# Kernel tuning notes

Measured on AMD Instinct MI355X. Metric: run time of the kernel, lower is better.

## Reference

```python
import jax, jax.numpy as jnp
import numpy as np

EPS = 1e-6     # vnn repo EPS used in VN nonlinearity / batchnorm norm
BN_EPS = 1e-5  # torch BatchNorm default eps
K = 40         # args.n_knn


def knn_idx(x, k):
    # x: (B, 3, N) -> (B, N, k) indices of k nearest neighbors (incl. self)
    inner = -2.0 * jnp.einsum('bdn,bdm->bnm', x, x)
    xx = jnp.sum(x * x, axis=1)  # (B, N)
    neg_dist = -xx[:, :, None] - inner - xx[:, None, :]
    _, idx = jax.lax.top_k(neg_dist, k)
    return idx


def get_graph_feature_cross(x, k):
    # x: (B, 3, N) -> (B, 3, 3, N, k): channels are [nbr - ctr, ctr, cross(nbr, ctr)]
    pts = jnp.transpose(x, (0, 2, 1))  # (B, N, 3)
    idx = knn_idx(x, k)                # (B, N, k)
    nbr = jax.vmap(lambda p, i: p[i])(pts, idx)          # (B, N, k, 3)
    ctr = jnp.broadcast_to(pts[:, :, None, :], nbr.shape)
    cross = jnp.cross(nbr, ctr)
    feat = jnp.stack([nbr - ctr, ctr, cross], axis=3)    # (B, N, k, 3, 3)
    return jnp.transpose(feat, (0, 3, 4, 1, 2))          # (B, C=3, 3vec, N, k)


def vn_bn(x):
    # VNBatchNorm (training-mode batch stats, affine = identity at init)
    # x: (B, C, 3, *rest); normalize the per-vector norm across (B, *rest)
    norm = jnp.sqrt(jnp.sum(x * x, axis=2)) + EPS  # (B, C, *rest)
    axes = (0,) + tuple(range(2, norm.ndim))
    mean = jnp.mean(norm, axis=axes, keepdims=True)
    var = jnp.var(norm, axis=axes, keepdims=True)
    norm_bn = (norm - mean) / jnp.sqrt(var + BN_EPS)
    return x / jnp.expand_dims(norm, 2) * jnp.expand_dims(norm_bn, 2)


def vn_lin(W, x):
    # channel-wise linear on axis 1 of (B, C, 3, ...)
    return jnp.einsum('oc,bc...->bo...', W, x)


def vn_lrelu(x, Wf, Wd):
    # VNLinearLeakyReLU with negative_slope=0.0
    p = vn_bn(vn_lin(Wf, x))
    d = vn_lin(Wd, x)
    dot = jnp.sum(p * d, axis=2, keepdims=True)
    dsq = jnp.sum(d * d, axis=2, keepdims=True)
    neg = p - (dot / (dsq + EPS)) * d  # project out the d component
    return jnp.where(dot >= 0, p, neg)


def vn_max_pool(x, W):
    # pool over last axis, picking the element maximizing <x, d> per (B, C, n)
    d = vn_lin(W, x)
    dot = jnp.sum(x * d, axis=2, keepdims=True)          # (B, C, 1, ..., K)
    idx = jnp.argmax(dot, axis=-1, keepdims=True)        # (B, C, 1, ..., 1)
    idx = jnp.broadcast_to(idx, x.shape[:-1] + (1,))
    return jnp.take_along_axis(x, idx, axis=-1)[..., 0]


def setup_inputs() -> dict:
    key = jax.random.key(0)
    ks = jax.random.split(key, 16)
    def w(k, o, i):
        bound = 1.0 / np.sqrt(i)  # torch nn.Linear default init
        return jax.random.uniform(k, (o, i), jnp.float32, -bound, bound)
    B, N = 8, 2048
    C1, C2, C3 = 64 // 3, 128 // 3, 1024 // 3  # 21, 42, 341
    F1, F2 = 512 // 3, 256 // 3                # 170, 85
    return {
        'x': jax.random.normal(ks[0], (B, 3, N), jnp.float32),
        'W_pos_feat': w(ks[1], C1, 3), 'W_pos_dir': w(ks[2], C1, 3),
        'W_gpool': w(ks[3], C1, C1),
        'W1_feat': w(ks[4], C1, C1), 'W1_dir': w(ks[5], C1, C1),
        'W2_feat': w(ks[6], C2, C1), 'W2_dir': w(ks[7], C2, C1),
        'W3_feat': w(ks[8], C3, C2), 'W3_dir': w(ks[9], C3, C2),
        'W_pool': w(ks[10], C3, C3),
        'Wf1_feat': w(ks[11], F1, C3), 'Wf1_dir': w(ks[12], F1, C3),
        'Wf2_feat': w(ks[13], F2, F1), 'Wf2_dir': w(ks[14], F2, F1),
        'Wf3': w(ks[15], 3, F2),
    }


def reference(x, W_pos_feat, W_pos_dir, W_gpool, W1_feat, W1_dir, W2_feat, W2_dir,
              W3_feat, W3_dir, W_pool, Wf1_feat, Wf1_dir, Wf2_feat, Wf2_dir, Wf3):
    feat = get_graph_feature_cross(x, K)            # (B, 3, 3, N, K)
    h = vn_lrelu(feat, W_pos_feat, W_pos_dir)       # (B, 21, 3, N, K)
    h = vn_max_pool(h, W_gpool)                     # (B, 21, 3, N)
    h = vn_lrelu(h, W1_feat, W1_dir)                # (B, 21, 3, N)
    h = vn_lrelu(h, W2_feat, W2_dir)                # (B, 42, 3, N)
    h = vn_lrelu(h, W3_feat, W3_dir)                # (B, 341, 3, N)
    h = vn_max_pool(h, W_pool)                      # (B, 341, 3)
    h = vn_lrelu(h, Wf1_feat, Wf1_dir)              # (B, 170, 3)
    h = vn_lrelu(h, Wf2_feat, Wf2_dir)              # (B, 85, 3)
    return vn_lin(Wf3, h)                           # (B, 3, 3)
```

## Files before the change

### kernel.cpp

```cpp
#include <hip/hip_runtime.h>

#define NP 2048
#define BATCH 8
#define KNN 40
#define EPSF 1e-6f
#define BNEPS 1e-5f

typedef __attribute__((ext_vector_type(8))) short short8;
typedef __attribute__((ext_vector_type(4))) float f32x4;

__device__ __forceinline__ unsigned ordf(float v){
  unsigned u = __float_as_uint(v);
  return (u & 0x80000000u) ? ~u : (u | 0x80000000u);
}

__device__ __forceinline__ void bsplit(float v, unsigned short &h, unsigned short &l){
  unsigned u = __float_as_uint(v);
  unsigned hu = (u + 0x7fffu + ((u >> 16) & 1u)) >> 16;
  h = (unsigned short)hu;
  float r = v - __uint_as_float(hu << 16);
  unsigned u2 = __float_as_uint(r);
  l = (unsigned short)((u2 + 0x7fffu + ((u2 >> 16) & 1u)) >> 16);
}

__device__ __forceinline__ float bf2f(unsigned short h){
  return __uint_as_float(((unsigned)h) << 16);
}

__global__ __launch_bounds__(256) void knn_kernel(const float* __restrict__ x, int* __restrict__ idx){
  __shared__ float4 sP[NP];
  int tid = threadIdx.x;
  int w = tid >> 6, lane = tid & 63;
  int row0 = blockIdx.x * 8 + w * 2, row1 = row0 + 1;
  int b = row0 >> 11;
  int i0 = row0 & 2047, i1 = row1 & 2047;
  const float* xb = x + b * 3 * NP;
  for (int t = tid; t < NP; t += 256){
    float a = xb[t], c = xb[NP + t], d = xb[2*NP + t];
    float xx = __fadd_rn(__fadd_rn(__fmul_rn(a,a), __fmul_rn(c,c)), __fmul_rn(d,d));
    sP[t] = make_float4(a, c, d, xx);
  }
  __syncthreads();
  float4 pa = sP[i0];
  float4 pb = sP[i1];
  const float4* lp = &sP[lane];
  unsigned long long a0 = 0, a1 = 0, a2 = 0, a3 = 0;
  unsigned long long b0 = 0, b1 = 0, b2 = 0, b3 = 0;
  #pragma unroll
  for (int m = 0; m < 32; m++){
    float4 pj = lp[m * 64];
    unsigned lowbits = (unsigned)(2047 - (m*64 + lane));
    float dotA = __fadd_rn(__fadd_rn(__fmul_rn(pa.x, pj.x), __fmul_rn(pa.y, pj.y)), __fmul_rn(pa.z, pj.z));
    float vA = __fsub_rn(__fsub_rn(-pa.w, __fmul_rn(-2.f, dotA)), pj.w);
    unsigned long long pkA = ((unsigned long long)ordf(vA) << 32) | lowbits;
    if (pkA > a3){
      if (pkA > a2){ a3 = a2; if (pkA > a1){ a2 = a1; if (pkA > a0){ a1 = a0; a0 = pkA; } else a1 = pkA; } else a2 = pkA; }
      else a3 = pkA;
    }
    float dotB = __fadd_rn(__fadd_rn(__fmul_rn(pb.x, pj.x), __fmul_rn(pb.y, pj.y)), __fmul_rn(pb.z, pj.z));
    float vB = __fsub_rn(__fsub_rn(-pb.w, __fmul_rn(-2.f, dotB)), pj.w);
    unsigned long long pkB = ((unsigned long long)ordf(vB) << 32) | lowbits;
    if (pkB > b3){
      if (pkB > b2){ b3 = b2; if (pkB > b1){ b2 = b1; if (pkB > b0){ b1 = b0; b0 = pkB; } else b1 = pkB; } else b2 = pkB; }
      else b3 = pkB;
    }
  }
  unsigned outA = 0, outB = 0;
  unsigned long long lastA = ~0ull, lastB = ~0ull;
  for (int kk = 0; kk < KNN; kk++){
    unsigned hvA = (unsigned)(a0 >> 32), hvB = (unsigned)(b0 >> 32);
    unsigned vmA = hvA, vmB = hvB;
    #pragma unroll
    for (int st = 32; st > 0; st >>= 1){
      unsigned oA = (unsigned)__shfl_xor((int)vmA, st, 64);
      unsigned oB = (unsigned)__shfl_xor((int)vmB, st, 64);
      vmA = (oA > vmA) ? oA : vmA;
      vmB = (oB > vmB) ? oB : vmB;
    }
    bool cA = (hvA == vmA), cB = (hvB == vmB);
    unsigned long long mA = __ballot(cA), mB = __ballot(cB);
    unsigned loA, loB;
    if (__popcll(mA) == 1){
      int wl = __ffsll((unsigned long long)mA) - 1;
      loA = (unsigned)__shfl((int)(unsigned)a0, wl, 64);
    } else {
      unsigned cl = cA ? (unsigned)a0 : 0u;
      #pragma unroll
      for (int st = 32; st > 0; st >>= 1){
        unsigned o = (unsigned)__shfl_xor((int)cl, st, 64);
        cl = (o > cl) ? o : cl;
      }
      loA = cl;
    }
    if (__popcll(mB) == 1){
      int wl = __ffsll((unsigned long long)mB) - 1;
      loB = (unsigned)__shfl((int)(unsigned)b0, wl, 64);
    } else {
      unsigned cl = cB ? (unsigned)b0 : 0u;
      #pragma unroll
      for (int st = 32; st > 0; st >>= 1){
        unsigned o = (unsigned)__shfl_xor((int)cl, st, 64);
        cl = (o > cl) ? o : cl;
      }
      loB = cl;
    }
    if (lane == kk){ outA = loA; outB = loB; }
    if (cA && (unsigned)a0 == loA){
      lastA = a0;
      a0 = a1; a1 = a2; a2 = a3; a3 = 0;
      if (a0 == 0){
        unsigned long long best = 0;
        #pragma unroll
        for (int m = 0; m < 32; m++){
          float4 pj = lp[m * 64];
          float dot = __fadd_rn(__fadd_rn(__fmul_rn(pa.x, pj.x), __fmul_rn(pa.y, pj.y)), __fmul_rn(pa.z, pj.z));
          float vv = __fsub_rn(__fsub_rn(-pa.w, __fmul_rn(-2.f, dot)), pj.w);
          unsigned long long pk = ((unsigned long long)ordf(vv) << 32) | (unsigned)(2047 - (m*64 + lane));
          if (pk < lastA && pk > best) best = pk;
        }
        a0 = best;
      }
    }
    if (cB && (unsigned)b0 == loB){
      lastB = b0;
      b0 = b1; b1 = b2; b2 = b3; b3 = 0;
      if (b0 == 0){
        unsigned long long best = 0;
        #pragma unroll
        for (int m = 0; m < 32; m++){
          float4 pj = lp[m * 64];
          float dot = __fadd_rn(__fadd_rn(__fmul_rn(pb.x, pj.x), __fmul_rn(pb.y, pj.y)), __fmul_rn(pb.z, pj.z));
          float vv = __fsub_rn(__fsub_rn(-pb.w, __fmul_rn(-2.f, dot)), pj.w);
          unsigned long long pk = ((unsigned long long)ordf(vv) << 32) | (unsigned)(2047 - (m*64 + lane));
          if (pk < lastB && pk > best) best = pk;
        }
        b0 = best;
      }
    }
  }
  if (lane < KNN){
    idx[row0 * KNN + lane] = 2047 - (int)outA;
    idx[row1 * KNN + lane] = 2047 - (int)outB;
  }
}

__global__ __launch_bounds__(256) void gf_stats(const float* __restrict__ x, const int* __restrict__ idx,
                                                const float* __restrict__ Wf, double* __restrict__ sums){
  int tid0 = blockIdx.x * 256 + threadIdx.x;
  float s[21], q[21];
  #pragma unroll
  for (int o = 0; o < 21; o++){ s[o] = 0.f; q[o] = 0.f; }
  for (int pix = tid0; pix < BATCH * NP * KNN; pix += 256 * 256){
    int rem = pix / KNN;
    int n = rem & 2047, b = rem >> 11;
    int j = idx[pix];
    const float* xb = x + b * 3 * NP;
    float c0 = xb[n], c1 = xb[NP + n], c2 = xb[2*NP + n];
    float a0 = xb[j], a1 = xb[NP + j], a2 = xb[2*NP + j];
    float r0 = a0 - c0, r1 = a1 - c1, r2 = a2 - c2;
    float g0 = a1*c2 - a2*c1, g1 = a2*c0 - a0*c2, g2 = a0*c1 - a1*c0;
    #pragma unroll
    for (int o = 0; o < 21; o++){
      float w0 = Wf[o*3], w1 = Wf[o*3+1], w2 = Wf[o*3+2];
      float p0 = w0*r0 + w1*c0 + w2*g0;
      float p1 = w0*r1 + w1*c1 + w2*g1;
      float p2 = w0*r2 + w1*c2 + w2*g2;
      float nm = sqrtf(p0*p0 + p1*p1 + p2*p2) + EPSF;
      s[o] += nm; q[o] += nm * nm;
    }
  }
  __shared__ float bs[4][42];
  int w = threadIdx.x >> 6;
  #pragma unroll
  for (int o = 0; o < 21; o++){
    float a = s[o], bb = q[o];
    #pragma unroll
    for (int st = 1; st < 64; st <<= 1){ a += __shfl_xor(a, st, 64); bb += __shfl_xor(bb, st, 64); }
    if ((threadIdx.x & 63) == 0){ bs[w][o] = a; bs[w][21 + o] = bb; }
  }
  __syncthreads();
  if (threadIdx.x < 42){
    float tot = bs[0][threadIdx.x] + bs[1][threadIdx.x] + bs[2][threadIdx.x] + bs[3][threadIdx.x];
    int o = threadIdx.x % 21, sq = threadIdx.x / 21;
    atomicAdd(&sums[2*o + sq], (double)tot);
  }
}

__global__ __launch_bounds__(320) void gf_applypool3(const float* __restrict__ x, const int* __restrict__ idx,
    const float* __restrict__ Wf, const float* __restrict__ Wd, const float* __restrict__ Wg,
    const float* __restrict__ mi, unsigned long long* __restrict__ packedGF){
  __shared__ unsigned long long sM[8*21];
  const int tid = threadIdx.x;
  for (int t = tid; t < 168; t += 320) sM[t] = 0ull;
  __syncthreads();
  const int pxl = tid / 40, k = tid - pxl * 40;
  const int px = blockIdx.x * 8 + pxl;
  const int b = px >> 11, n = px & 2047;
  const float* xb = x + b * 3 * NP;
  float c0 = xb[n], c1 = xb[NP + n], c2 = xb[2*NP + n];
  int j = idx[(size_t)px * KNN + k];
  float a0 = xb[j], a1 = xb[NP + j], a2 = xb[2*NP + j];
  float r0 = a0 - c0, r1 = a1 - c1, r2 = a2 - c2;
  float g0 = a1*c2 - a2*c1, g1 = a2*c0 - a0*c2, g2 = a0*c1 - a1*c0;
  float h[21][3];
  #pragma unroll
  for (int o = 0; o < 21; o++){
    float w0 = Wf[o*3], w1 = Wf[o*3+1], w2 = Wf[o*3+2];
    float p0 = w0*r0 + w1*c0 + w2*g0;
    float p1 = w0*r1 + w1*c1 + w2*g1;
    float p2 = w0*r2 + w1*c2 + w2*g2;
    float nm = sqrtf(p0*p0 + p1*p1 + p2*p2) + EPSF;
    float f = (nm - mi[2*o]) * mi[2*o+1] / nm;
    p0 *= f; p1 *= f; p2 *= f;
    float v0 = Wd[o*3], v1 = Wd[o*3+1], v2 = Wd[o*3+2];
    float d0 = v0*r0 + v1*c0 + v2*g0;
    float d1 = v0*r1 + v1*c1 + v2*g1;
    float d2 = v0*r2 + v1*c2 + v2*g2;
    float dot = p0*d0 + p1*d1 + p2*d2;
    float dsq = d0*d0 + d1*d1 + d2*d2;
    float t = dot / (dsq + EPSF);
    h[o][0] = (dot >= 0.f) ? p0 : fmaf(-t, d0, p0);
    h[o][1] = (dot >= 0.f) ? p1 : fmaf(-t, d1, p1);
    h[o][2] = (dot >= 0.f) ? p2 : fmaf(-t, d2, p2);
  }
  #pragma unroll
  for (int o = 0; o < 21; o++){
    float q0 = 0.f, q1 = 0.f, q2 = 0.f;
    #pragma unroll
    for (int c = 0; c < 21; c++){
      float wg = Wg[o*21 + c];
      q0 = fmaf(wg, h[c][0], q0); q1 = fmaf(wg, h[c][1], q1); q2 = fmaf(wg, h[c][2], q2);
    }
    float dp = q0*h[o][0] + q1*h[o][1] + q2*h[o][2];
    unsigned long long pk = ((unsigned long long)ordf(dp) << 32) | (unsigned)(63 - k);
    atomicMax(&sM[pxl*21 + o], pk);
  }
  __syncthreads();
  for (int t = tid; t < 168; t += 320){
    int lpx = t / 21, lo = t - lpx * 21;
    packedGF[(size_t)(blockIdx.x * 8 + lpx) * 21 + lo] = sM[t];
  }
}

__global__ __launch_bounds__(256) void gf_gather(const float* __restrict__ x, const int* __restrict__ idx,
    const float* __restrict__ Wf, const float* __restrict__ Wd, const float* __restrict__ mi,
    const unsigned long long* __restrict__ packedGF, float* __restrict__ h1){
  int t = blockIdx.x * 256 + threadIdx.x;
  if (t >= BATCH * NP * 21) return;
  int px = t / 21, o = t - px * 21;
  int b = px >> 11, n = px & 2047;
  int k = 63 - (int)(packedGF[t] & 0xffffffffu);
  int j = idx[(size_t)px * KNN + k];
  const float* xb = x + b * 3 * NP;
  float c0 = xb[n], c1 = xb[NP + n], c2 = xb[2*NP + n];
  float a0 = xb[j], a1 = xb[NP + j], a2 = xb[2*NP + j];
  float r0 = a0 - c0, r1 = a1 - c1, r2 = a2 - c2;
  float g0 = a1*c2 - a2*c1, g1 = a2*c0 - a0*c2, g2 = a0*c1 - a1*c0;
  float w0 = Wf[o*3], w1 = Wf[o*3+1], w2 = Wf[o*3+2];
  float p0 = w0*r0 + w1*c0 + w2*g0;
  float p1 = w0*r1 + w1*c1 + w2*g1;
  float p2 = w0*r2 + w1*c2 + w2*g2;
  float nm = sqrtf(p0*p0 + p1*p1 + p2*p2) + EPSF;
  float f = (nm - mi[2*o]) * mi[2*o+1] / nm;
  p0 *= f; p1 *= f; p2 *= f;
  float v0 = Wd[o*3], v1 = Wd[o*3+1], v2 = Wd[o*3+2];
  float d0 = v0*r0 + v1*c0 + v2*g0;
  float d1 = v0*r1 + v1*c1 + v2*g1;
  float d2 = v0*r2 + v1*c2 + v2*g2;
  float dot = p0*d0 + p1*d1 + p2*d2;
  float dsq = d0*d0 + d1*d1 + d2*d2;
  float tt = dot / (dsq + EPSF);
  float o0 = (dot >= 0.f) ? p0 : fmaf(-tt, d0, p0);
  float o1 = (dot >= 0.f) ? p1 : fmaf(-tt, d1, p1);
  float o2 = (dot >= 0.f) ? p2 : fmaf(-tt, d2, p2);
  float* dst = h1 + (size_t)((b*21 + o)*3) * NP + n;
  dst[0] = o0; dst[NP] = o1; dst[2*NP] = o2;
}

template<int CIN>
__global__ __launch_bounds__(256) void layer_stats2(const float* __restrict__ hin, const float* __restrict__ Wf,
                                                    double* __restrict__ sums, int Co){
  const int px0 = blockIdx.x * 1024;
  const int b = px0 >> 11;
  const int n0 = (px0 & 2047) + (threadIdx.x << 2);
  const int o0 = blockIdx.y * 8;
  const float* hb = hin + (size_t)b * CIN * 3 * NP + n0;
  float p[8][3][4];
  #pragma unroll
  for (int oo = 0; oo < 8; oo++)
    #pragma unroll
    for (int e = 0; e < 3; e++)
      #pragma unroll
      for (int k = 0; k < 4; k++) p[oo][e][k] = 0.f;
  for (int c = 0; c < CIN; c++){
    float4 hv[3];
    #pragma unroll
    for (int e = 0; e < 3; e++) hv[e] = *(const float4*)&hb[(size_t)(c*3 + e) * NP];
    #pragma unroll
    for (int oo = 0; oo < 8; oo++){
      int o = o0 + oo; if (o >= Co) o = Co - 1;
      float wv = Wf[o*CIN + c];
      #pragma unroll
      for (int e = 0; e < 3; e++){
        p[oo][e][0] = fmaf(wv, hv[e].x, p[oo][e][0]);
        p[oo][e][1] = fmaf(wv, hv[e].y, p[oo][e][1]);
        p[oo][e][2] = fmaf(wv, hv[e].z, p[oo][e][2]);
        p[oo][e][3] = fmaf(wv, hv[e].w, p[oo][e][3]);
      }
    }
  }
  float sl[8], ql[8];
  #pragma unroll
  for (int oo = 0; oo < 8; oo++){
    sl[oo] = 0.f; ql[oo] = 0.f;
    #pragma unroll
    for (int k = 0; k < 4; k++){
      float nm = sqrtf(p[oo][0][k]*p[oo][0][k] + p[oo][1][k]*p[oo][1][k] + p[oo][2][k]*p[oo][2][k]) + EPSF;
      sl[oo] += nm; ql[oo] += nm * nm;
    }
  }
  __shared__ float red[4][16];
  int w = threadIdx.x >> 6;
  #pragma unroll
  for (int oo = 0; oo < 8; oo++){
    float sv = sl[oo], qv = ql[oo];
    #pragma unroll
    for (int st = 1; st < 64; st <<= 1){ sv += __shfl_xor(sv, st, 64); qv += __shfl_xor(qv, st, 64); }
    if ((threadIdx.x & 63) == 0){ red[w][oo] = sv; red[w][8 + oo] = qv; }
  }
  __syncthreads();
  if (threadIdx.x < 16){
    float tot = red[0][threadIdx.x] + red[1][threadIdx.x] + red[2][threadIdx.x] + red[3][threadIdx.x];
    int oo = threadIdx.x & 7, isq = threadIdx.x >> 3;
    int o = o0 + oo;
    if (o < Co) atomicAdd(&sums[2*o + isq], (double)tot);
  }
}

template<int CIN>
__global__ __launch_bounds__(256) void layer_apply2(const float* __restrict__ hin, const float* __restrict__ Wf,
    const float* __restrict__ Wd, const float* __restrict__ mi, float* __restrict__ hout, int Co){
  const int px = blockIdx.x * 256 + threadIdx.x;
  const int b = px >> 11, n = px & 2047;
  const int o0 = blockIdx.y * 8;
  const float* hb = hin + (size_t)b * CIN * 3 * NP + n;
  float p[8][3], d[8][3];
  #pragma unroll
  for (int oo = 0; oo < 8; oo++)
    #pragma unroll
    for (int e = 0; e < 3; e++){ p[oo][e] = 0.f; d[oo][e] = 0.f; }
  for (int c = 0; c < CIN; c++){
    float h0 = hb[(size_t)(c*3 + 0) * NP];
    float h1 = hb[(size_t)(c*3 + 1) * NP];
    float h2 = hb[(size_t)(c*3 + 2) * NP];
    #pragma unroll
    for (int oo = 0; oo < 8; oo++){
      int o = o0 + oo; if (o >= Co) o = Co - 1;
      float wf = Wf[o*CIN + c], wd = Wd[o*CIN + c];
      p[oo][0] = fmaf(wf, h0, p[oo][0]); p[oo][1] = fmaf(wf, h1, p[oo][1]); p[oo][2] = fmaf(wf, h2, p[oo][2]);
      d[oo][0] = fmaf(wd, h0, d[oo][0]); d[oo][1] = fmaf(wd, h1, d[oo][1]); d[oo][2] = fmaf(wd, h2, d[oo][2]);
    }
  }
  #pragma unroll
  for (int oo = 0; oo < 8; oo++){
    int o = o0 + oo;
    if (o < Co){
      float nm = sqrtf(p[oo][0]*p[oo][0] + p[oo][1]*p[oo][1] + p[oo][2]*p[oo][2]) + EPSF;
      float f = (nm - mi[2*o]) * mi[2*o+1] / nm;
      float p0 = p[oo][0]*f, p1 = p[oo][1]*f, p2 = p[oo][2]*f;
      float dot = p0*d[oo][0] + p1*d[oo][1] + p2*d[oo][2];
      float dsq = d[oo][0]*d[oo][0] + d[oo][1]*d[oo][1] + d[oo][2]*d[oo][2];
      float t = dot / (dsq + EPSF);
      float r0 = (dot >= 0.f) ? p0 : fmaf(-t, d[oo][0], p0);
      float r1 = (dot >= 0.f) ? p1 : fmaf(-t, d[oo][1], p1);
      float r2 = (dot >= 0.f) ? p2 : fmaf(-t, d[oo][2], p2);
      float* dst = hout + (size_t)((b*Co + o)*3) * NP + n;
      dst[0] = r0; dst[NP] = r1; dst[2*NP] = r2;
    }
  }
}

__global__ __launch_bounds__(256) void layer_apply2_k(const float* __restrict__ hin, const float* __restrict__ Wf,
    const float* __restrict__ Wd, const float* __restrict__ mi,
    unsigned short* __restrict__ Hk3h, unsigned short* __restrict__ Hk3l){
  const int px = blockIdx.x * 256 + threadIdx.x;
  const int b = px >> 11, n = px & 2047;
  const int kb = blockIdx.y;
  const float* hb = hin + (size_t)b * 21 * 3 * NP + n;
  float r[8][3];
  #pragma unroll
  for (int oo = 0; oo < 8; oo++)
    #pragma unroll
    for (int e = 0; e < 3; e++) r[oo][e] = 0.f;
  if (kb < 6){
    float p[8][3], d[8][3];
    #pragma unroll
    for (int oo = 0; oo < 8; oo++)
      #pragma unroll
      for (int e = 0; e < 3; e++){ p[oo][e] = 0.f; d[oo][e] = 0.f; }
    for (int c = 0; c < 21; c++){
      float h0 = hb[(size_t)(c*3 + 0) * NP];
      float h1 = hb[(size_t)(c*3 + 1) * NP];
      float h2 = hb[(size_t)(c*3 + 2) * NP];
      #pragma unroll
      for (int oo = 0; oo < 8; oo++){
        int o = kb*8 + oo; if (o >= 42) o = 41;
        float wf = Wf[o*21 + c], wd = Wd[o*21 + c];
        p[oo][0] = fmaf(wf, h0, p[oo][0]); p[oo][1] = fmaf(wf, h1, p[oo][1]); p[oo][2] = fmaf(wf, h2, p[oo][2]);
        d[oo][0] = fmaf(wd, h0, d[oo][0]); d[oo][1] = fmaf(wd, h1, d[oo][1]); d[oo][2] = fmaf(wd, h2, d[oo][2]);
      }
    }
    #pragma unroll
    for (int oo = 0; oo < 8; oo++){
      int o = kb*8 + oo;
      if (o < 42){
        float nm = sqrtf(p[oo][0]*p[oo][0] + p[oo][1]*p[oo][1] + p[oo][2]*p[oo][2]) + EPSF;
        float f = (nm - mi[2*o]) * mi[2*o+1] / nm;
        float p0 = p[oo][0]*f, p1 = p[oo][1]*f, p2 = p[oo][2]*f;
        float dot = p0*d[oo][0] + p1*d[oo][1] + p2*d[oo][2];
        float dsq = d[oo][0]*d[oo][0] + d[oo][1]*d[oo][1] + d[oo][2]*d[oo][2];
        float t = dot / (dsq + EPSF);
        r[oo][0] = (dot >= 0.f) ? p0 : fmaf(-t, d[oo][0], p0);
        r[oo][1] = (dot >= 0.f) ? p1 : fmaf(-t, d[oo][1], p1);
        r[oo][2] = (dot >= 0.f) ? p2 : fmaf(-t, d[oo][2], p2);
      }
    }
  }
  #pragma unroll
  for (int e = 0; e < 3; e++){
    unsigned ph[4], pl[4];
    #pragma unroll
    for (int oo = 0; oo < 8; oo++){
      unsigned short hh, ll;
      bsplit(r[oo][e], hh, ll);
      if (!(oo & 1)){ ph[oo>>1] = hh; pl[oo>>1] = ll; }
      else { ph[oo>>1] |= ((unsigned)hh) << 16; pl[oo>>1] |= ((unsigned)ll) << 16; }
    }
    size_t base = ((((size_t)(b*3 + e))*8 + kb) * 2048 + n) * 8;
    *(uint4*)(Hk3h + base) = make_uint4(ph[0], ph[1], ph[2], ph[3]);
    *(uint4*)(Hk3l + base) = make_uint4(pl[0], pl[1], pl[2], pl[3]);
  }
}

__global__ void finalize_stats(const double* __restrict__ sums, float* __restrict__ mi, int Co, double invM){
  int o = blockIdx.x * 64 + threadIdx.x;
  if (o >= Co) return;
  double m = sums[2*o] * invM;
  double v = sums[2*o+1] * invM - m * m;
  if (v < 0.0) v = 0.0;
  mi[2*o] = (float)m;
  mi[2*o+1] = (float)(1.0 / sqrt(v + (double)BNEPS));
}

__global__ __launch_bounds__(256) void wk_kernel(const float* __restrict__ Wp,
    unsigned short* __restrict__ Wkh, unsigned short* __restrict__ Wkl){
  int t = blockIdx.x * 256 + threadIdx.x;
  if (t >= 44*384*8) return;
  int j = t & 7, o = (t >> 3) % 384, cb = t / (384*8);
  int c = cb*8 + j;
  float v = (c < 341 && o < 341) ? Wp[o*341 + c] : 0.f;
  unsigned short h, l;
  bsplit(v, h, l);
  Wkh[t] = h; Wkl[t] = l;
}

__global__ __launch_bounds__(256) void wk3_kernel(const float* __restrict__ W3f, const float* __restrict__ W3d,
    unsigned short* __restrict__ Wfh, unsigned short* __restrict__ Wfl,
    unsigned short* __restrict__ Wdh, unsigned short* __restrict__ Wdl){
  int t = blockIdx.x * 256 + threadIdx.x;
  if (t >= 8*384*8) return;
  int j = t & 7, o = (t >> 3) % 384, cb = t / (384*8);
  int c = cb*8 + j;
  bool ok = (c < 42 && o < 341);
  float vf = ok ? W3f[o*42 + c] : 0.f;
  float vd = ok ? W3d[o*42 + c] : 0.f;
  unsigned short h, l;
  bsplit(vf, h, l); Wfh[t] = h; Wfl[t] = l;
  bsplit(vd, h, l); Wdh[t] = h; Wdl[t] = l;
}

__global__ __launch_bounds__(256) void stats3_mfma(const unsigned short* __restrict__ Wfh,
    const unsigned short* __restrict__ Wfl, const unsigned short* __restrict__ Hh,
    const unsigned short* __restrict__ Hl, double* __restrict__ sums){
  __shared__ unsigned short sB[2][8][64][8];
  const int b = blockIdx.z, o0 = blockIdx.y * 64, n0 = blockIdx.x * 64;
  const int t = threadIdx.x, w = t >> 6, l = t & 63;
  const int r = l & 15, g = l >> 4;
  const int wo = o0 + w * 16;
  const int skb = t >> 5, sn = (t & 31) * 2;
  f32x4 acc[3][4];
  #pragma unroll
  for (int e = 0; e < 3; e++)
    #pragma unroll
    for (int nt = 0; nt < 4; nt++) acc[e][nt] = (f32x4)0.f;
  for (int e = 0; e < 3; e++){
    if (e) __syncthreads();
    const uint4* srcH = (const uint4*)(Hh + ((((size_t)(b*3 + e))*8 + skb) * 2048 + n0 + sn) * 8);
    const uint4* srcL = (const uint4*)(Hl + ((((size_t)(b*3 + e))*8 + skb) * 2048 + n0 + sn) * 8);
    uint4 h0 = srcH[0], h1 = srcH[1], l0 = srcL[0], l1 = srcL[1];
    *(uint4*)&sB[0][skb][sn][0] = h0; *(uint4*)&sB[0][skb][sn+1][0] = h1;
    *(uint4*)&sB[1][skb][sn][0] = l0; *(uint4*)&sB[1][skb][sn+1][0] = l1;
    __syncthreads();
    #pragma unroll
    for (int kt = 0; kt < 2; kt++){
      size_t aoff = (((size_t)(kt*4 + g)) * 384 + wo + r) * 8;
      short8 ah = *(const short8*)(Wfh + aoff);
      short8 al = *(const short8*)(Wfl + aoff);
      #pragma unroll
      for (int nt = 0; nt < 4; nt++){
        short8 bh = *(const short8*)&sB[0][kt*4 + g][nt*16 + r][0];
        short8 bl = *(const short8*)&sB[1][kt*4 + g][nt*16 + r][0];
        acc[e][nt] = __builtin_amdgcn_mfma_f32_16x16x32_bf16(ah, bh, acc[e][nt], 0, 0, 0);
        acc[e][nt] = __builtin_amdgcn_mfma_f32_16x16x32_bf16(ah, bl, acc[e][nt], 0, 0, 0);
        acc[e][nt] = __builtin_amdgcn_mfma_f32_16x16x32_bf16(al, bh, acc[e][nt], 0, 0, 0);
      }
    }
  }
  #pragma unroll
  for (int jj = 0; jj < 4; jj++){
    int o = wo + g*4 + jj;
    float s1 = 0.f, s2 = 0.f;
    #pragma unroll
    for (int nt = 0; nt < 4; nt++){
      float p0 = acc[0][nt][jj], p1 = acc[1][nt][jj], p2 = acc[2][nt][jj];
      float nm = sqrtf(p0*p0 + p1*p1 + p2*p2) + EPSF;
      s1 += nm; s2 += nm * nm;
    }
    #pragma unroll
    for (int st = 1; st < 16; st <<= 1){
      s1 += __shfl_xor(s1, st, 64);
      s2 += __shfl_xor(s2, st, 64);
    }
    if (r == 0 && o < 341){
      atomicAdd(&sums[2*o], (double)s1);
      atomicAdd(&sums[2*o+1], (double)s2);
    }
  }
}

__global__ __launch_bounds__(256) void apply3_mfma(const unsigned short* __restrict__ Wfh,
    const unsigned short* __restrict__ Wfl, const unsigned short* __restrict__ Wdh,
    const unsigned short* __restrict__ Wdl, const unsigned short* __restrict__ Hh,
    const unsigned short* __restrict__ Hl, const float* __restrict__ mi,
    unsigned short* __restrict__ Hkh, unsigned short* __restrict__ Hkl){
  __shared__ unsigned short sB[2][8][64][8];
  const int b = blockIdx.z, o0 = blockIdx.y * 64, n0 = blockIdx.x * 64;
  const int t = threadIdx.x, w = t >> 6, l = t & 63;
  const int r = l & 15, g = l >> 4;
  const int wo = o0 + w * 16;
  const int skb = t >> 5, sn = (t & 31) * 2;
  f32x4 accp[3][4], accd[3][4];
  #pragma unroll
  for (int e = 0; e < 3; e++)
    #pragma unroll
    for (int nt = 0; nt < 4; nt++){ accp[e][nt] = (f32x4)0.f; accd[e][nt] = (f32x4)0.f; }
  for (int e = 0; e < 3; e++){
    if (e) __syncthreads();
    const uint4* srcH = (const uint4*)(Hh + ((((size_t)(b*3 + e))*8 + skb) * 2048 + n0 + sn) * 8);
    const uint4* srcL = (const uint4*)(Hl + ((((size_t)(b*3 + e))*8 + skb) * 2048 + n0 + sn) * 8);
    uint4 h0 = srcH[0], h1 = srcH[1], l0 = srcL[0], l1 = srcL[1];
    *(uint4*)&sB[0][skb][sn][0] = h0; *(uint4*)&sB[0][skb][sn+1][0] = h1;
    *(uint4*)&sB[1][skb][sn][0] = l0; *(uint4*)&sB[1][skb][sn+1][0] = l1;
    __syncthreads();
    #pragma unroll
    for (int kt = 0; kt < 2; kt++){
      size_t aoff = (((size_t)(kt*4 + g)) * 384 + wo + r) * 8;
      short8 afh = *(const short8*)(Wfh + aoff);
      short8 afl = *(const short8*)(Wfl + aoff);
      short8 adh = *(const short8*)(Wdh + aoff);
      short8 adl = *(const short8*)(Wdl + aoff);
      #pragma unroll
      for (int nt = 0; nt < 4; nt++){
        short8 bh = *(const short8*)&sB[0][kt*4 + g][nt*16 + r][0];
        short8 bl = *(const short8*)&sB[1][kt*4 + g][nt*16 + r][0];
        accp[e][nt] = __builtin_amdgcn_mfma_f32_16x16x32_bf16(afh, bh, accp[e][nt], 0, 0, 0);
        accp[e][nt] = __builtin_amdgcn_mfma_f32_16x16x32_bf16(afh, bl, accp[e][nt], 0, 0, 0);
        accp[e][nt] = __builtin_amdgcn_mfma_f32_16x16x32_bf16(afl, bh, accp[e][nt], 0, 0, 0);
        accd[e][nt] = __builtin_amdgcn_mfma_f32_16x16x32_bf16(adh, bh, accd[e][nt], 0, 0, 0);
        accd[e][nt] = __builtin_amdgcn_mfma_f32_16x16x32_bf16(adh, bl, accd[e][nt], 0, 0, 0);
        accd[e][nt] = __builtin_amdgcn_mfma_f32_16x16x32_bf16(adl, bh, accd[e][nt], 0, 0, 0);
      }
    }
  }
  const int obase = wo + g*4;
  const int kb = obase >> 3, jo = obase & 7;
  #pragma unroll
  for (int nt = 0; nt < 4; nt++){
    float rr[3][4];
    #pragma unroll
    for (int jj = 0; jj < 4; jj++){
      int o = obase + jj;
      float r0 = 0.f, r1 = 0.f, r2 = 0.f;
      if (o < 341){
        float p0 = accp[0][nt][jj], p1 = accp[1][nt][jj], p2 = accp[2][nt][jj];
        float d0 = accd[0][nt][jj], d1 = accd[1][nt][jj], d2 = accd[2][nt][jj];
        float nm = sqrtf(p0*p0 + p1*p1 + p2*p2) + EPSF;
        float f = (nm - mi[2*o]) * mi[2*o+1] / nm;
        p0 *= f; p1 *= f; p2 *= f;
        float dot = p0*d0 + p1*d1 + p2*d2;
        float dsq = d0*d0 + d1*d1 + d2*d2;
        float tt = dot / (dsq + EPSF);
        r0 = (dot >= 0.f) ? p0 : fmaf(-tt, d0, p0);
        r1 = (dot >= 0.f) ? p1 : fmaf(-tt, d1, p1);
        r2 = (dot >= 0.f) ? p2 : fmaf(-tt, d2, p2);
      }
      rr[0][jj] = r0; rr[1][jj] = r1; rr[2][jj] = r2;
    }
    int n = n0 + nt*16 + r;
    #pragma unroll
    for (int e = 0; e < 3; e++){
      unsigned short h0, l0, h1, l1, h2, l2, h3, l3;
      bsplit(rr[e][0], h0, l0); bsplit(rr[e][1], h1, l1);
      bsplit(rr[e][2], h2, l2); bsplit(rr[e][3], h3, l3);
      unsigned ph0 = (unsigned)h0 | ((unsigned)h1 << 16);
      unsigned ph1 = (unsigned)h2 | ((unsigned)h3 << 16);
      unsigned pl0 = (unsigned)l0 | ((unsigned)l1 << 16);
      unsigned pl1 = (unsigned)l2 | ((unsigned)l3 << 16);
      size_t base = ((((size_t)(b*3 + e))*48 + kb) * 2048 + (size_t)n) * 8 + jo;
      *(uint2*)(Hkh + base) = make_uint2(ph0, ph1);
      *(uint2*)(Hkl + base) = make_uint2(pl0, pl1);
    }
  }
}

__global__ __launch_bounds__(256) void pool_mfma(const unsigned short* __restrict__ Wkh,
    const unsigned short* __restrict__ Wkl, const unsigned short* __restrict__ Hkh,
    const unsigned short* __restrict__ Hkl, unsigned long long* __restrict__ packed){
  __shared__ unsigned short sB[2][2][4][64][8];
  const int b = blockIdx.z, o0 = blockIdx.y * 128, n0 = blockIdx.x * 64;
  const int t = threadIdx.x, w = t >> 6, l = t & 63;
  const int wo = o0 + w * 32;
  const int r = l & 15, g = l >> 4;
  const int skb = t >> 6, sn = t & 63;
  const int ktw = wo >> 5;

  f32x4 acc[2][4], dotv[2][4], hval[2][4];
  #pragma unroll
  for (int s = 0; s < 2; s++)
    #pragma unroll
    for (int nt = 0; nt < 4; nt++){ dotv[s][nt] = (f32x4)0.f; hval[s][nt] = (f32x4)0.f; }

  auto gsrc = [&](const unsigned short* base, int e, int kt) -> const uint4* {
    return (const uint4*)(base + ((((size_t)(b*3 + e))*48 + (size_t)(kt*4 + skb)) * 2048 + n0 + sn) * 8);
  };

  uint4 rg[2];
  rg[0] = *gsrc(Hkh, 0, 0);
  rg[1] = *gsrc(Hkl, 0, 0);

  for (int ek = 0; ek < 33; ek++){
    const int e = ek / 11, kt = ek - e*11, buf = ek & 1;
    *(uint4*)&sB[buf][0][skb][sn][0] = rg[0];
    *(uint4*)&sB[buf][1][skb][sn][0] = rg[1];
    __syncthreads();
    if (ek < 32){
      int e2 = (ek+1) / 11, kt2 = (ek+1) - e2*11;
      rg[0] = *gsrc(Hkh, e2, kt2);
      rg[1] = *gsrc(Hkl, e2, kt2);
    }
    if (kt == 0){
      #pragma unroll
      for (int s = 0; s < 2; s++)
        #pragma unroll
        for (int nt = 0; nt < 4; nt++) acc[s][nt] = (f32x4)0.f;
    }
    short8 ah[2], al[2];
    #pragma unroll
    for (int s = 0; s < 2; s++){
      size_t aoff = (((size_t)(kt*4 + g)) * 384 + (wo + s*16 + r)) * 8;
      ah[s] = *(const short8*)(Wkh + aoff);
      al[s] = *(const short8*)(Wkl + aoff);
    }
    #pragma unroll
    for (int nt = 0; nt < 4; nt++){
      short8 bh = *(const short8*)&sB[buf][0][g][nt*16 + r][0];
      short8 bl = *(const short8*)&sB[buf][1][g][nt*16 + r][0];
      #pragma unroll
      for (int s = 0; s < 2; s++){
        acc[s][nt] = __builtin_amdgcn_mfma_f32_16x16x32_bf16(ah[s], bh, acc[s][nt], 0, 0, 0);
        acc[s][nt] = __builtin_amdgcn_mfma_f32_16x16x32_bf16(ah[s], bl, acc[s][nt], 0, 0, 0);
        acc[s][nt] = __builtin_amdgcn_mfma_f32_16x16x32_bf16(al[s], bh, acc[s][nt], 0, 0, 0);
      }
    }
    if (kt == ktw){
      #pragma unroll
      for (int s = 0; s < 2; s++){
        #pragma unroll
        for (int jj = 0; jj < 4; jj++){
          int oin = s*16 + g*4 + jj;
          #pragma unroll
          for (int nt = 0; nt < 4; nt++){
            hval[s][nt][jj] = bf2f(sB[buf][0][oin>>3][nt*16 + r][oin&7])
                            + bf2f(sB[buf][1][oin>>3][nt*16 + r][oin&7]);
          }
        }
      }
    }
    __syncthreads();
    if (kt == 10){
      #pragma unroll
      for (int s = 0; s < 2; s++)
        #pragma unroll
        for (int nt = 0; nt < 4; nt++)
          #pragma unroll
          for (int jj = 0; jj < 4; jj++)
            dotv[s][nt][jj] += acc[s][nt][jj] * hval[s][nt][jj];
    }
  }
  #pragma unroll
  for (int s = 0; s < 2; s++){
    #pragma unroll
    for (int j = 0; j < 4; j++){
      int o = wo + s*16 + g*4 + j;
      unsigned long long best = 0;
      #pragma unroll
      for (int nt = 0; nt < 4; nt++){
        int n = n0 + nt*16 + r;
        unsigned long long pk = ((unsigned long long)ordf(dotv[s][nt][j]) << 32) | (unsigned)(2047 - n);
        if (pk > best) best = pk;
      }
      #pragma unroll
      for (int st = 1; st < 16; st <<= 1){
        unsigned long long ob = __shfl_xor(best, st, 64);
        if (ob > best) best = ob;
      }
      if (r == 0 && o < 341) atomicMax(&packed[b*341 + o], best);
    }
  }
}

__global__ void pool_gather(const unsigned long long* __restrict__ packed,
                            const unsigned short* __restrict__ Hkh, const unsigned short* __restrict__ Hkl,
                            float* __restrict__ pooled){
  int t = blockIdx.x * 256 + threadIdx.x;
  if (t >= BATCH * 341) return;
  int n = 2047 - (int)(packed[t] & 0xffffffffu);
  int b = t / 341, o = t % 341;
  #pragma unroll
  for (int e = 0; e < 3; e++){
    size_t hb = ((((size_t)(b*3 + e))*48 + (o >> 3)) * 2048 + n) * 8 + (o & 7);
    pooled[t*3 + e] = bf2f(Hkh[hb]) + bf2f(Hkl[hb]);
  }
}

__global__ __launch_bounds__(64) void flayer(const float* __restrict__ in, const float* __restrict__ Wf,
    const float* __restrict__ Wd, float* __restrict__ out, int Cin, int Co){
  int o = blockIdx.x, lane = threadIdx.x;
  float pv[24], dv[24];
  #pragma unroll
  for (int be = 0; be < 24; be++){ pv[be] = 0.f; dv[be] = 0.f; }
  for (int c = lane; c < Cin; c += 64){
    float wf = Wf[o*Cin + c], wd = Wd[o*Cin + c];
    #pragma unroll
    for (int bb = 0; bb < 8; bb++){
      #pragma unroll
      for (int e = 0; e < 3; e++){
        float hv = in[(bb*Cin + c)*3 + e];
        pv[bb*3+e] = fmaf(wf, hv, pv[bb*3+e]);
        dv[bb*3+e] = fmaf(wd, hv, dv[bb*3+e]);
      }
    }
  }
  #pragma unroll
  for (int be = 0; be < 24; be++){
    #pragma unroll
    for (int st = 1; st < 64; st <<= 1){
      pv[be] += __shfl_xor(pv[be], st, 64);
      dv[be] += __shfl_xor(dv[be], st, 64);
    }
  }
  float nm[8], dotb[8], dsqb[8];
  float mean = 0.f;
  #pragma unroll
  for (int bb = 0; bb < 8; bb++){
    nm[bb] = sqrtf(pv[bb*3]*pv[bb*3] + pv[bb*3+1]*pv[bb*3+1] + pv[bb*3+2]*pv[bb*3+2]) + EPSF;
    mean += nm[bb];
  }
  mean *= 0.125f;
  float var = 0.f;
  #pragma unroll
  for (int bb = 0; bb < 8; bb++){ float dvv = nm[bb] - mean; var += dvv * dvv; }
  var *= 0.125f;
  float istd = 1.f / sqrtf(var + BNEPS);
  #pragma unroll
  for (int bb = 0; bb < 8; bb++){
    float f = (nm[bb] - mean) * istd / nm[bb];
    dotb[bb] = f * (pv[bb*3]*dv[bb*3] + pv[bb*3+1]*dv[bb*3+1] + pv[bb*3+2]*dv[bb*3+2]);
    dsqb[bb] = dv[bb*3]*dv[bb*3] + dv[bb*3+1]*dv[bb*3+1] + dv[bb*3+2]*dv[bb*3+2];
  }
  #pragma unroll
  for (int be = 0; be < 24; be++){
    if (lane == be){
      int bb = be / 3;
      float f = (nm[bb] - mean) * istd / nm[bb];
      float pe = pv[be] * f;
      float t = dotb[bb] / (dsqb[bb] + EPSF);
      float res = (dotb[bb] >= 0.f) ? pe : fmaf(-t, dv[be], pe);
      out[(bb*Co + o)*3 + (be % 3)] = res;
    }
  }
}

__global__ void final_lin(const float* __restrict__ in, const float* __restrict__ W, float* __restrict__ out){
  int t = threadIdx.x;
  if (t >= 72) return;
  int b = t / 9, o = (t % 9) / 3, e = t % 3;
  float s = 0.f;
  for (int c = 0; c < 85; c++) s = fmaf(W[o*85 + c], in[(b*85 + c)*3 + e], s);
  out[t] = s;
}

extern "C" void kernel_launch(void* const* d_in, const int* in_sizes, int n_in,
                              void* d_out, int out_size, void* d_ws, size_t ws_size,
                              hipStream_t stream){
  const float* x   = (const float*)d_in[0];
  const float* Wpf = (const float*)d_in[1];
  const float* Wpd = (const float*)d_in[2];
  const float* Wg  = (const float*)d_in[3];
  const float* W1f = (const float*)d_in[4];
  const float* W1d = (const float*)d_in[5];
  const float* W2f = (const float*)d_in[6];
  const float* W2d = (const float*)d_in[7];
  const float* W3f = (const float*)d_in[8];
  const float* W3d = (const float*)d_in[9];
  const float* Wpool = (const float*)d_in[10];
  const float* Wf1f = (const float*)d_in[11];
  const float* Wf1d = (const float*)d_in[12];
  const float* Wf2f = (const float*)d_in[13];
  const float* Wf2d = (const float*)d_in[14];
  const float* Wf3  = (const float*)d_in[15];
  float* out = (float*)d_out;

  char* ws = (char*)d_ws;
  size_t off = 0;
  int*   idx  = (int*)(ws + off);             off += (size_t)BATCH*NP*KNN*4;
  unsigned long long* packedGF = (unsigned long long*)(ws + off); off += (size_t)BATCH*NP*21*8;
  float* h1  = (float*)(ws + off);            off += (size_t)BATCH*21*3*NP*4;
  float* h2  = (float*)(ws + off);            off += (size_t)BATCH*21*3*NP*4;
  unsigned short* Hk3h = (unsigned short*)(ws + off); off += (size_t)BATCH*3*8*NP*8*2;
  unsigned short* Hk3l = (unsigned short*)(ws + off); off += (size_t)BATCH*3*8*NP*8*2;
  unsigned short* Hkh = (unsigned short*)(ws + off); off += (size_t)BATCH*3*48*NP*8*2;
  unsigned short* Hkl = (unsigned short*)(ws + off); off += (size_t)BATCH*3*48*NP*8*2;
  unsigned short* Wkh = (unsigned short*)(ws + off); off += (size_t)44*384*8*2;
  unsigned short* Wkl = (unsigned short*)(ws + off); off += (size_t)44*384*8*2;
  unsigned short* Wk3fh = (unsigned short*)(ws + off); off += (size_t)8*384*8*2;
  unsigned short* Wk3fl = (unsigned short*)(ws + off); off += (size_t)8*384*8*2;
  unsigned short* Wk3dh = (unsigned short*)(ws + off); off += (size_t)8*384*8*2;
  unsigned short* Wk3dl = (unsigned short*)(ws + off); off += (size_t)8*384*8*2;
  char*  zbase = ws + off;
  double* sums_gf = (double*)(ws + off);      off += 8192;
  double* sums_l1 = (double*)(ws + off);      off += 8192;
  double* sums_l2 = (double*)(ws + off);      off += 8192;
  double* sums_l3 = (double*)(ws + off);      off += 8192;
  unsigned long long* packed = (unsigned long long*)(ws + off); off += 24576;
  size_t zbytes = (ws + off) - zbase;
  float* mi_gf = (float*)(ws + off);          off += 1024;
  float* mi_l1 = (float*)(ws + off);          off += 1024;
  float* mi_l2 = (float*)(ws + off);          off += 1024;
  float* mi_l3 = (float*)(ws + off);          off += 4096;
  float* pooled = (float*)(ws + off);         off += (size_t)BATCH*341*3*4 + 32;
  float* h5 = (float*)(ws + off);             off += (size_t)BATCH*170*3*4 + 32;
  float* h6 = (float*)(ws + off);             off += (size_t)BATCH*85*3*4 + 32;

  hipMemsetAsync(zbase, 0, zbytes, stream);

  knn_kernel<<<BATCH*NP/8, 256, 0, stream>>>(x, idx);
  wk_kernel<<<(44*384*8 + 255)/256, 256, 0, stream>>>(Wpool, Wkh, Wkl);
  wk3_kernel<<<(8*384*8 + 255)/256, 256, 0, stream>>>(W3f, W3d, Wk3fh, Wk3fl, Wk3dh, Wk3dl);

  gf_stats<<<256, 256, 0, stream>>>(x, idx, Wpf, sums_gf);
  finalize_stats<<<1, 64, 0, stream>>>(sums_gf, mi_gf, 21, 1.0 / (double)(BATCH*NP*KNN));
  gf_applypool3<<<BATCH*NP/8, 320, 0, stream>>>(x, idx, Wpf, Wpd, Wg, mi_gf, packedGF);
  gf_gather<<<(BATCH*NP*21 + 255)/256, 256, 0, stream>>>(x, idx, Wpf, Wpd, mi_gf, packedGF, h1);

  layer_stats2<21><<<dim3(16,3), 256, 0, stream>>>(h1, W1f, sums_l1, 21);
  finalize_stats<<<1, 64, 0, stream>>>(sums_l1, mi_l1, 21, 1.0 / (double)(BATCH*NP));
  layer_apply2<21><<<dim3(64,3), 256, 0, stream>>>(h1, W1f, W1d, mi_l1, h2, 21);

  layer_stats2<21><<<dim3(16,6), 256, 0, stream>>>(h2, W2f, sums_l2, 42);
  finalize_stats<<<1, 64, 0, stream>>>(sums_l2, mi_l2, 42, 1.0 / (double)(BATCH*NP));
  layer_apply2_k<<<dim3(64,8), 256, 0, stream>>>(h2, W2f, W2d, mi_l2, Hk3h, Hk3l);

  stats3_mfma<<<dim3(32, 6, BATCH), 256, 0, stream>>>(Wk3fh, Wk3fl, Hk3h, Hk3l, sums_l3);
  finalize_stats<<<6, 64, 0, stream>>>(sums_l3, mi_l3, 341, 1.0 / (double)(BATCH*NP));
  apply3_mfma<<<dim3(32, 6, BATCH), 256, 0, stream>>>(Wk3fh, Wk3fl, Wk3dh, Wk3dl, Hk3h, Hk3l, mi_l3, Hkh, Hkl);

  pool_mfma<<<dim3(32, 3, BATCH), 256, 0, stream>>>(Wkh, Wkl, Hkh, Hkl, packed);
  pool_gather<<<(BATCH*341 + 255)/256, 256, 0, stream>>>(packed, Hkh, Hkl, pooled);

  flayer<<<170, 64, 0, stream>>>(pooled, Wf1f, Wf1d, h5, 341, 170);
  flayer<<<85, 64, 0, stream>>>(h5, Wf2f, Wf2d, h6, 170, 85);
  final_lin<<<1, 128, 0, stream>>>(h6, Wf3, out);
}
```

Baseline: 469.9 us.

## Fuse graph-feature gather into pool kernel and halve pool_mfma output tile

After the shared-memory argmax in gf_applypool3, the thread whose neighbor index matches the winning tag writes its already-computed h values straight to h1. This removes the separate gf_gather kernel, the packedGF buffer, and the recomputation of the winning element. Separately, pool_mfma now has each wave cover 16 output channels instead of 32, with twice as many blocks along y. That gives more parallelism and fewer registers per thread, at the cost of reloading the B tiles from shared memory twice as often.

After: 520.6 us. 1.11x slower.

```diff
diff --git a/kernel.cpp b/kernel.cpp
--- a/kernel.cpp
+++ b/kernel.cpp
@@ -188,7 +188,7 @@
 
 __global__ __launch_bounds__(320) void gf_applypool3(const float* __restrict__ x, const int* __restrict__ idx,
     const float* __restrict__ Wf, const float* __restrict__ Wd, const float* __restrict__ Wg,
-    const float* __restrict__ mi, unsigned long long* __restrict__ packedGF){
+    const float* __restrict__ mi, float* __restrict__ h1){
   __shared__ unsigned long long sM[8*21];
   const int tid = threadIdx.x;
   for (int t = tid; t < 168; t += 320) sM[t] = 0ull;
@@ -236,45 +236,14 @@
     atomicMax(&sM[pxl*21 + o], pk);
   }
   __syncthreads();
-  for (int t = tid; t < 168; t += 320){
-    int lpx = t / 21, lo = t - lpx * 21;
-    packedGF[(size_t)(blockIdx.x * 8 + lpx) * 21 + lo] = sM[t];
-  }
-}
-
-__global__ __launch_bounds__(256) void gf_gather(const float* __restrict__ x, const int* __restrict__ idx,
-    const float* __restrict__ Wf, const float* __restrict__ Wd, const float* __restrict__ mi,
-    const unsigned long long* __restrict__ packedGF, float* __restrict__ h1){
-  int t = blockIdx.x * 256 + threadIdx.x;
-  if (t >= BATCH * NP * 21) return;
-  int px = t / 21, o = t - px * 21;
-  int b = px >> 11, n = px & 2047;
-  int k = 63 - (int)(packedGF[t] & 0xffffffffu);
-  int j = idx[(size_t)px * KNN + k];
-  const float* xb = x + b * 3 * NP;
-  float c0 = xb[n], c1 = xb[NP + n], c2 = xb[2*NP + n];
-  float a0 = xb[j], a1 = xb[NP + j], a2 = xb[2*NP + j];
-  float r0 = a0 - c0, r1 = a1 - c1, r2 = a2 - c2;
-  float g0 = a1*c2 - a2*c1, g1 = a2*c0 - a0*c2, g2 = a0*c1 - a1*c0;
-  float w0 = Wf[o*3], w1 = Wf[o*3+1], w2 = Wf[o*3+2];
-  float p0 = w0*r0 + w1*c0 + w2*g0;
-  float p1 = w0*r1 + w1*c1 + w2*g1;
-  float p2 = w0*r2 + w1*c2 + w2*g2;
-  float nm = sqrtf(p0*p0 + p1*p1 + p2*p2) + EPSF;
-  float f = (nm - mi[2*o]) * mi[2*o+1] / nm;
-  p0 *= f; p1 *= f; p2 *= f;
-  float v0 = Wd[o*3], v1 = Wd[o*3+1], v2 = Wd[o*3+2];
-  float d0 = v0*r0 + v1*c0 + v2*g0;
-  float d1 = v0*r1 + v1*c1 + v2*g1;
-  float d2 = v0*r2 + v1*c2 + v2*g2;
-  float dot = p0*d0 + p1*d1 + p2*d2;
-  float dsq = d0*d0 + d1*d1 + d2*d2;
-  float tt = dot / (dsq + EPSF);
-  float o0 = (dot >= 0.f) ? p0 : fmaf(-tt, d0, p0);
-  float o1 = (dot >= 0.f) ? p1 : fmaf(-tt, d1, p1);
-  float o2 = (dot >= 0.f) ? p2 : fmaf(-tt, d2, p2);
-  float* dst = h1 + (size_t)((b*21 + o)*3) * NP + n;
-  dst[0] = o0; dst[NP] = o1; dst[2*NP] = o2;
+  const unsigned mytag = (unsigned)(63 - k);
+  #pragma unroll
+  for (int o = 0; o < 21; o++){
+    if ((unsigned)(sM[pxl*21 + o] & 0xffffffffu) == mytag){
+      float* dst = h1 + (size_t)((b*21 + o)*3) * NP + n;
+      dst[0] = h[o][0]; dst[NP] = h[o][1]; dst[2*NP] = h[o][2];
+    }
+  }
 }
 
 template<int CIN>
@@ -627,18 +596,16 @@
     const unsigned short* __restrict__ Wkl, const unsigned short* __restrict__ Hkh,
     const unsigned short* __restrict__ Hkl, unsigned long long* __restrict__ packed){
   __shared__ unsigned short sB[2][2][4][64][8];
-  const int b = blockIdx.z, o0 = blockIdx.y * 128, n0 = blockIdx.x * 64;
+  const int b = blockIdx.z, o0 = blockIdx.y * 64, n0 = blockIdx.x * 64;
   const int t = threadIdx.x, w = t >> 6, l = t & 63;
-  const int wo = o0 + w * 32;
+  const int wo = o0 + w * 16;
   const int r = l & 15, g = l >> 4;
   const int skb = t >> 6, sn = t & 63;
   const int ktw = wo >> 5;
 
-  f32x4 acc[2][4], dotv[2][4], hval[2][4];
-  #pragma unroll
-  for (int s = 0; s < 2; s++)
-    #pragma unroll
-    for (int nt = 0; nt < 4; nt++){ dotv[s][nt] = (f32x4)0.f; hval[s][nt] = (f32x4)0.f; }
+  f32x4 acc[4], dotv[4], hval[4];
+  #pragma unroll
+  for (int nt = 0; nt < 4; nt++){ dotv[nt] = (f32x4)0.f; hval[nt] = (f32x4)0.f; }
 
   auto gsrc = [&](const unsigned short* base, int e, int kt) -> const uint4* {
     return (const uint4*)(base + ((((size_t)(b*3 + e))*48 + (size_t)(kt*4 + skb)) * 2048 + n0 + sn) * 8);
@@ -660,72 +627,55 @@
     }
     if (kt == 0){
       #pragma unroll
-      for (int s = 0; s < 2; s++)
-        #pragma unroll
-        for (int nt = 0; nt < 4; nt++) acc[s][nt] = (f32x4)0.f;
-    }
-    short8 ah[2], al[2];
-    #pragma unroll
-    for (int s = 0; s < 2; s++){
-      size_t aoff = (((size_t)(kt*4 + g)) * 384 + (wo + s*16 + r)) * 8;
-      ah[s] = *(const short8*)(Wkh + aoff);
-      al[s] = *(const short8*)(Wkl + aoff);
-    }
+      for (int nt = 0; nt < 4; nt++) acc[nt] = (f32x4)0.f;
+    }
+    size_t aoff = (((size_t)(kt*4 + g)) * 384 + (wo + r)) * 8;
+    short8 ah = *(const short8*)(Wkh + aoff);
+    short8 al = *(const short8*)(Wkl + aoff);
     #pragma unroll
     for (int nt = 0; nt < 4; nt++){
       short8 bh = *(const short8*)&sB[buf][0][g][nt*16 + r][0];
       short8 bl = *(const short8*)&sB[buf][1][g][nt*16 + r][0];
-      #pragma unroll
-      for (int s = 0; s < 2; s++){
-        acc[s][nt] = __builtin_amdgcn_mfma_f32_16x16x32_bf16(ah[s], bh, acc[s][nt], 0, 0, 0);
-        acc[s][nt] = __builtin_amdgcn_mfma_f32_16x16x32_bf16(ah[s], bl, acc[s][nt], 0, 0, 0);
-        acc[s][nt] = __builtin_amdgcn_mfma_f32_16x16x32_bf16(al[s], bh, acc[s][nt], 0, 0, 0);
-      }
+      acc[nt] = __builtin_amdgcn_mfma_f32_16x16x32_bf16(ah, bh, acc[nt], 0, 0, 0);
+      acc[nt] = __builtin_amdgcn_mfma_f32_16x16x32_bf16(ah, bl, acc[nt], 0, 0, 0);
+      acc[nt] = __builtin_amdgcn_mfma_f32_16x16x32_bf16(al, bh, acc[nt], 0, 0, 0);
     }
     if (kt == ktw){
       #pragma unroll
-      for (int s = 0; s < 2; s++){
+      for (int jj = 0; jj < 4; jj++){
+        int oin = (wo & 31) + g*4 + jj;
         #pragma unroll
-        for (int jj = 0; jj < 4; jj++){
-          int oin = s*16 + g*4 + jj;
-          #pragma unroll
-          for (int nt = 0; nt < 4; nt++){
-            hval[s][nt][jj] = bf2f(sB[buf][0][oin>>3][nt*16 + r][oin&7])
-                            + bf2f(sB[buf][1][oin>>3][nt*16 + r][oin&7]);
-          }
+        for (int nt = 0; nt < 4; nt++){
+          hval[nt][jj] = bf2f(sB[buf][0][oin>>3][nt*16 + r][oin&7])
+                       + bf2f(sB[buf][1][oin>>3][nt*16 + r][oin&7]);
         }
       }
     }
     __syncthreads();
     if (kt == 10){
       #pragma unroll
-      for (int s = 0; s < 2; s++)
+      for (int nt = 0; nt < 4; nt++)
         #pragma unroll
-        for (int nt = 0; nt < 4; nt++)
-          #pragma unroll
-          for (int jj = 0; jj < 4; jj++)
-            dotv[s][nt][jj] += acc[s][nt][jj] * hval[s][nt][jj];
-    }
-  }
-  #pragma unroll
-  for (int s = 0; s < 2; s++){
-    #pragma unroll
-    for (int j = 0; j < 4; j++){
-      int o = wo + s*16 + g*4 + j;
-      unsigned long long best = 0;
-      #pragma unroll
-      for (int nt = 0; nt < 4; nt++){
-        int n = n0 + nt*16 + r;
-        unsigned long long pk = ((unsigned long long)ordf(dotv[s][nt][j]) << 32) | (unsigned)(2047 - n);
-        if (pk > best) best = pk;
-      }
-      #pragma unroll
-      for (int st = 1; st < 16; st <<= 1){
-        unsigned long long ob = __shfl_xor(best, st, 64);
-        if (ob > best) best = ob;
-      }
-      if (r == 0 && o < 341) atomicMax(&packed[b*341 + o], best);
-    }
+        for (int jj = 0; jj < 4; jj++)
+          dotv[nt][jj] += acc[nt][jj] * hval[nt][jj];
+    }
+  }
+  #pragma unroll
+  for (int j = 0; j < 4; j++){
+    int o = wo + g*4 + j;
+    unsigned long long best = 0;
+    #pragma unroll
+    for (int nt = 0; nt < 4; nt++){
+      int n = n0 + nt*16 + r;
+      unsigned long long pk = ((unsigned long long)ordf(dotv[nt][j]) << 32) | (unsigned)(2047 - n);
+      if (pk > best) best = pk;
+    }
+    #pragma unroll
+    for (int st = 1; st < 16; st <<= 1){
+      unsigned long long ob = __shfl_xor(best, st, 64);
+      if (ob > best) best = ob;
+    }
+    if (r == 0 && o < 341) atomicMax(&packed[b*341 + o], best);
   }
 }
 
@@ -834,7 +784,6 @@
   char* ws = (char*)d_ws;
   size_t off = 0;
   int*   idx  = (int*)(ws + off);             off += (size_t)BATCH*NP*KNN*4;
-  unsigned long long* packedGF = (unsigned long long*)(ws + off); off += (size_t)BATCH*NP*21*8;
   float* h1  = (float*)(ws + off);            off += (size_t)BATCH*21*3*NP*4;
   float* h2  = (float*)(ws + off);            off += (size_t)BATCH*21*3*NP*4;
   unsigned short* Hk3h = (unsigned short*)(ws + off); off += (size_t)BATCH*3*8*NP*8*2;
@@ -870,8 +819,7 @@
 
   gf_stats<<<256, 256, 0, stream>>>(x, idx, Wpf, sums_gf);
   finalize_stats<<<1, 64, 0, stream>>>(sums_gf, mi_gf, 21, 1.0 / (double)(BATCH*NP*KNN));
-  gf_applypool3<<<BATCH*NP/8, 320, 0, stream>>>(x, idx, Wpf, Wpd, Wg, mi_gf, packedGF);
-  gf_gather<<<(BATCH*NP*21 + 255)/256, 256, 0, stream>>>(x, idx, Wpf, Wpd, mi_gf, packedGF, h1);
+  gf_applypool3<<<BATCH*NP/8, 320, 0, stream>>>(x, idx, Wpf, Wpd, Wg, mi_gf, h1);
 
   layer_stats2<21><<<dim3(16,3), 256, 0, stream>>>(h1, W1f, sums_l1, 21);
   finalize_stats<<<1, 64, 0, stream>>>(sums_l1, mi_l1, 21, 1.0 / (double)(BATCH*NP));
@@ -885,7 +833,7 @@
   finalize_stats<<<6, 64, 0, stream>>>(sums_l3, mi_l3, 341, 1.0 / (double)(BATCH*NP));
   apply3_mfma<<<dim3(32, 6, BATCH), 256, 0, stream>>>(Wk3fh, Wk3fl, Wk3dh, Wk3dl, Hk3h, Hk3l, mi_l3, Hkh, Hkl);
 
-  pool_mfma<<<dim3(32, 3, BATCH), 256, 0, stream>>>(Wkh, Wkl, Hkh, Hkl, packed);
+  pool_mfma<<<dim3(32, 6, BATCH), 256, 0, stream>>>(Wkh, Wkl, Hkh, Hkl, packed);
   pool_gather<<<(BATCH*341 + 255)/256, 256, 0, stream>>>(packed, Hkh, Hkl, pooled);
 
   flayer<<<170, 64, 0, stream>>>(pooled, Wf1f, Wf1d, h5, 341, 170);
```
